# Kernel optimization log

Hardware: AMD Instinct MI355X
Metric: run time of the kernel (lower is better)

Reference implementation:

```python
import jax, jax.numpy as jnp
import numpy as np
from jax.scipy.special import logsumexp

N, K, D = 131072, 256, 32


def setup_inputs() -> dict:
    key = jax.random.key(0)
    k1, k2, k3 = jax.random.split(key, 3)
    points = jax.random.normal(k1, (N, D), dtype=jnp.float32)
    centers = jax.random.uniform(k2, (K, D), dtype=jnp.float32)
    # well-conditioned inverse-sqrt covariances (original used 15*I; scaled to
    # avoid float32 overflow in sqrt(det(covs_inv)) for D=32)
    covs_inv_sqrt = (0.5 * jnp.broadcast_to(jnp.eye(D, dtype=jnp.float32), (K, D, D))
                     + 0.02 * jax.random.normal(k3, (K, D, D), dtype=jnp.float32))
    weights = jnp.ones((K,), dtype=jnp.float32)
    threshold = jnp.zeros((1,), dtype=jnp.float32)
    return {"points": points, "centers": centers,
            "covs_inv_sqrt": covs_inv_sqrt, "weights": weights,
            "threshold": threshold}


def reference(points, centers, covs_inv_sqrt, weights, threshold):
    # refresh(): equal_clusters=True branch
    w = jnp.abs(weights)
    center_prs = w / (w.sum() + 1e-30)                       # [K]
    covs_inv = jnp.einsum('kde,kfe->kdf', covs_inv_sqrt, covs_inv_sqrt)  # [K,D,D]
    coefs = center_prs * jnp.sqrt(jnp.linalg.det(covs_inv))  # [K]

    # pairwise weighted sqdist: q_ij = (x_i - c_j)^T A_j (x_i - c_j)
    B = covs_inv.reshape(K, D * D)                           # [K, D*D]
    X2 = (points[:, :, None] * points[:, None, :]).reshape(N, D * D)  # [N, D*D]
    t_xAx = X2 @ B.T                                         # [N, K]
    m = jnp.einsum('kde,ke->kd', covs_inv, centers)          # A_j c_j, [K,D]
    t_xAc = points @ m.T                                     # [N, K]
    t_cAc = jnp.einsum('kd,kd->k', m, centers)               # [K]
    d_ij = -0.5 * (t_xAx - 2.0 * t_xAc + t_cAc[None, :])     # [N, K]

    # weighted logsumexp over centers, then subtract threshold
    ll = logsumexp(d_ij, axis=1, b=coefs[None, :])           # [N]
    return ll[:, None] - threshold[0]                        # [N, 1]
```

## Files before the change

### kernel.cpp

```cpp
#include <hip/hip_runtime.h>
#include <math.h>

#define NPTS 131072
#define KCOMP 256
#define DIM 32
#define NREAL 560
#define NCH 18
#define PSIF_BYTES 294912
#define WS_NEED (PSIF_BYTES + KCOMP * 4)

typedef __attribute__((ext_vector_type(8))) short short8;
typedef __attribute__((ext_vector_type(16))) float f32x16;

__device__ __forceinline__ unsigned short f2bf(float v) {
    unsigned u = __float_as_uint(v);
    u += 0x7fffu + ((u >> 16) & 1u);
    return (unsigned short)(u >> 16);
}

__device__ __forceinline__ unsigned pkbf(float lo, float hi) {
#if __has_builtin(__builtin_amdgcn_perm)
    const unsigned a = __float_as_uint(hi) + 0x8000u;
    const unsigned b = __float_as_uint(lo) + 0x8000u;
    return __builtin_amdgcn_perm(a, b, 0x07060302u);
#else
    return (unsigned)f2bf(lo) | ((unsigned)f2bf(hi) << 16);
#endif
}

__device__ __forceinline__ void dma16(const uint4* g, uint4* s) {
    __builtin_amdgcn_global_load_lds(
        (const __attribute__((address_space(1))) void*)g,
        (__attribute__((address_space(3))) void*)s, 16, 0, 0);
}

constexpr int PfxT(int d) { return 32 * d - (d * (d - 1)) / 2; }
constexpr int rowT(int p) { int d = 0; while (d < 31 && PfxT(d + 1) <= p) ++d; return d; }
constexpr int colT(int p) { return rowT(p) + (p - PfxT(rowT(p))); }

template<int P, int J>
__device__ __forceinline__ float genOne(const float (&x)[DIM]) {
    constexpr int p = P + J;
    if constexpr (p >= NREAL) {
        return 0.f;
    } else if constexpr (p >= 528) {
        return x[p - 528];
    } else {
        constexpr int d = rowT(p);
        constexpr int f = colT(p);
        static_assert(d >= 0 && d < 32 && f >= d && f < 32, "bad feature map");
        return x[d] * x[f];
    }
}

__global__ __launch_bounds__(256) void gmm_pre(
    const float* __restrict__ S,
    const float* __restrict__ centers,
    const float* __restrict__ weights,
    unsigned short* __restrict__ PsiF,
    float* __restrict__ kc2)
{
    __shared__ float Sl[DIM][DIM + 1];
    __shared__ float As[DIM][DIM + 1];
    __shared__ float cl[DIM], ml[DIM];
    __shared__ float red[256];

    const int k = blockIdx.x, tid = threadIdx.x;

    for (int idx = tid; idx < DIM * DIM; idx += 256)
        Sl[idx >> 5][idx & 31] = S[(size_t)k * DIM * DIM + idx];
    if (tid < DIM) cl[tid] = centers[k * DIM + tid];
    __syncthreads();

    for (int idx = tid; idx < DIM * DIM; idx += 256) {
        const int d = idx >> 5, f = idx & 31;
        float a = 0.f;
#pragma unroll
        for (int e = 0; e < DIM; ++e) a = fmaf(Sl[d][e], Sl[f][e], a);
        As[d][f] = a;
    }
    __syncthreads();

    if (tid < DIM) {
        float mv = 0.f;
#pragma unroll
        for (int f = 0; f < DIM; ++f) mv = fmaf(As[tid][f], cl[f], mv);
        ml[tid] = mv;
    }
    __syncthreads();

    for (int p = tid; p < NREAL; p += 256) {
        float val;
        if (p < 528) {
            int d = 0, pr = 0;
            while (pr + (32 - d) <= p) { pr += (32 - d); ++d; }
            const int f = d + (p - pr);
            val = (f == d) ? -0.5f * As[d][d] : -As[d][f];
        } else {
            val = ml[p - 528];
        }
        const int c = p >> 6, kk = p & 63;
        const int s = kk >> 4, qq = (kk >> 3) & 1, j = kk & 7;
        const int ct = k >> 5, ll = qq * 32 + (k & 31);
        const int g = c * 2048 + (s * 8 + ct) * 64 + ll;
        PsiF[(size_t)g * 8 + j] = f2bf(val);
    }

    red[tid] = fabsf(weights[tid]);
    __syncthreads();
    for (int off = 128; off > 0; off >>= 1) {
        if (tid < off) red[tid] += red[tid + off];
        __syncthreads();
    }
    const float wsum = red[0];

    for (int j = 0; j < DIM - 1; ++j) {
        const float inv = 1.0f / As[j][j];
        for (int idx = tid; idx < DIM * DIM; idx += 256) {
            const int r = idx >> 5, c = idx & 31;
            if (r > j && c > j)
                As[r][c] = fmaf(-As[r][j] * inv, As[j][c], As[r][c]);
        }
        __syncthreads();
    }

    if (tid < DIM) red[tid] = __logf(As[tid][tid]);
    __syncthreads();
    if (tid == 0) {
        float sl = 0.f;
        for (int j = 0; j < DIM; ++j) sl += red[j];
        float cac = 0.f;
        for (int d2 = 0; d2 < DIM; ++d2) cac = fmaf(ml[d2], cl[d2], cac);
        kc2[k] = __logf(fabsf(weights[k])) - __logf(wsum + 1e-30f)
               + 0.5f * sl - 0.5f * cac;
    }
}

template<int P>
__device__ __forceinline__ void genQuad(const float (&x)[DIM], float* v) {
    v[0] = genOne<P, 0>(x);
    v[1] = genOne<P, 1>(x);
    v[2] = genOne<P, 2>(x);
    v[3] = genOne<P, 3>(x);
}

template<int CH, int SS>
__device__ __forceinline__ void genSite(const float (&x)[DIM], uint4* base,
                                        int rbg, int r32) {
    float v[8];
    genQuad<CH * 32 + SS * 8>(x, v);
    genQuad<CH * 32 + SS * 8 + 4>(x, v + 4);
    uint4 u;
    u.x = pkbf(v[0], v[1]);
    u.y = pkbf(v[2], v[3]);
    u.z = pkbf(v[4], v[5]);
    u.w = pkbf(v[6], v[7]);
    base[(SS >> 1) * 256 + rbg * 64 + (SS & 1) * 32 + r32] = u;
}

template<int CH>
__device__ __forceinline__ void genChunk(const float (&x)[DIM], uint4* sA4,
                                         int q, int rbg, int r32) {
    uint4* base = sA4 + (CH & 1) * 512;
    if (q == 0) {
        genSite<CH, 0>(x, base, rbg, r32);
        if constexpr (CH < 17) genSite<CH, 2>(x, base, rbg, r32);
    } else {
        genSite<CH, 1>(x, base, rbg, r32);
        if constexpr (CH < 17) genSite<CH, 3>(x, base, rbg, r32);
    }
}

template<int C>
__device__ __forceinline__ void doChunk(const float (&x)[DIM],
    uint4* sA4, uint4* sB4, const uint4* __restrict__ PsiF4,
    f32x16 (&acc0)[4], f32x16 (&acc1)[4],
    int l, int w, int q, int rbg, int r32, int r0, int c0)
{

    if constexpr (C + 1 < NCH) {
        constexpr int NI = (C + 1 == 17) ? 2 : 4;
        const uint4* src = PsiF4 + (C + 1) * 1024 + w * 64 + l;
        uint4* dst = sB4 + ((C + 1) & 1) * 1024 + w * 64 + l;
#pragma unroll
        for (int i = 0; i < NI; ++i) dma16(src + i * 256, dst + i * 256);
    }

    if constexpr (C + 1 < NCH) genChunk<C + 1>(x, sA4, q, rbg, r32);

    constexpr int NS = (C < 17) ? 2 : 1;
    const uint4* aa = sA4 + (C & 1) * 512;
    const uint4* bb = sB4 + (C & 1) * 1024;
#pragma unroll
    for (int s = 0; s < NS; ++s) {
        short8 a0 = __builtin_bit_cast(short8, aa[(s * 4 + r0) * 64 + l]);
        short8 a1 = __builtin_bit_cast(short8, aa[(s * 4 + r0 + 1) * 64 + l]);
#pragma unroll
        for (int j = 0; j < 4; ++j) {
            short8 b = __builtin_bit_cast(short8, bb[(s * 8 + c0 + j) * 64 + l]);
            acc0[j] = __builtin_amdgcn_mfma_f32_32x32x16_bf16(a0, b, acc0[j], 0, 0, 0);
            acc1[j] = __builtin_amdgcn_mfma_f32_32x32x16_bf16(a1, b, acc1[j], 0, 0, 0);
        }
    }

    __syncthreads();
}

__device__ __forceinline__ void epiHalf(const f32x16 (&acc)[4], const float (&kcv)[4],
    int rblock, int l, int whalf, float (*sM)[2], float (*sS)[2])
{
#pragma unroll
    for (int rg = 0; rg < 16; ++rg) {
        float vals[4], m = -INFINITY;
#pragma unroll
        for (int j = 0; j < 4; ++j) { vals[j] = acc[j][rg] + kcv[j]; m = fmaxf(m, vals[j]); }
#pragma unroll
        for (int mask = 1; mask < 32; mask <<= 1) m = fmaxf(m, __shfl_xor(m, mask, 64));
        float sv = 0.f;
#pragma unroll
        for (int j = 0; j < 4; ++j) sv += __expf(vals[j] - m);
#pragma unroll
        for (int mask = 1; mask < 32; mask <<= 1) sv += __shfl_xor(sv, mask, 64);
        if ((l & 31) == 0) {
            const int R = rblock * 32 + (rg & 3) + 8 * (rg >> 2) + 4 * (l >> 5);
            sM[R][whalf] = m; sS[R][whalf] = sv;
        }
    }
}

__global__ __launch_bounds__(256, 2) void gmm_mfma(
    const float* __restrict__ points,
    const unsigned short* __restrict__ PsiF,
    const float* __restrict__ kc2,
    const float* __restrict__ thr,
    float* __restrict__ out)
{
    __shared__ uint4 sA4[1024];
    __shared__ uint4 sB4[2048];
    float (*sM)[2] = (float (*)[2])sA4;
    float (*sS)[2] = (float (*)[2])(sA4 + 64);

    const int t = threadIdx.x;
    const int w = t >> 6, l = t & 63;
    const int row = t & 127, q = t >> 7;
    const int rbg = row >> 5, r32 = row & 31;
    const int r0 = (w >> 1) * 2, c0 = (w & 1) * 4;

    const uint4* PsiF4 = (const uint4*)PsiF;

    {
        const uint4* src = PsiF4 + w * 64 + l;
        uint4* dst = sB4 + w * 64 + l;
#pragma unroll
        for (int i = 0; i < 4; ++i) dma16(src + i * 256, dst + i * 256);
    }

    float x[DIM];
    const float4* px = (const float4*)(points + ((size_t)blockIdx.x * 128 + row) * DIM);
#pragma unroll
    for (int j2 = 0; j2 < 8; ++j2) {
        float4 v = px[j2];
        x[4 * j2 + 0] = v.x; x[4 * j2 + 1] = v.y;
        x[4 * j2 + 2] = v.z; x[4 * j2 + 3] = v.w;
    }

    f32x16 acc0[4], acc1[4];
#pragma unroll
    for (int j = 0; j < 4; ++j)
#pragma unroll
        for (int r = 0; r < 16; ++r) { acc0[j][r] = 0.f; acc1[j][r] = 0.f; }

    genChunk<0>(x, sA4, q, rbg, r32);
    __syncthreads();

    doChunk<0>(x, sA4, sB4, PsiF4, acc0, acc1, l, w, q, rbg, r32, r0, c0);
    doChunk<1>(x, sA4, sB4, PsiF4, acc0, acc1, l, w, q, rbg, r32, r0, c0);
    doChunk<2>(x, sA4, sB4, PsiF4, acc0, acc1, l, w, q, rbg, r32, r0, c0);
    doChunk<3>(x, sA4, sB4, PsiF4, acc0, acc1, l, w, q, rbg, r32, r0, c0);
    doChunk<4>(x, sA4, sB4, PsiF4, acc0, acc1, l, w, q, rbg, r32, r0, c0);
    doChunk<5>(x, sA4, sB4, PsiF4, acc0, acc1, l, w, q, rbg, r32, r0, c0);
    doChunk<6>(x, sA4, sB4, PsiF4, acc0, acc1, l, w, q, rbg, r32, r0, c0);
    doChunk<7>(x, sA4, sB4, PsiF4, acc0, acc1, l, w, q, rbg, r32, r0, c0);
    doChunk<8>(x, sA4, sB4, PsiF4, acc0, acc1, l, w, q, rbg, r32, r0, c0);
    doChunk<9>(x, sA4, sB4, PsiF4, acc0, acc1, l, w, q, rbg, r32, r0, c0);
    doChunk<10>(x, sA4, sB4, PsiF4, acc0, acc1, l, w, q, rbg, r32, r0, c0);
    doChunk<11>(x, sA4, sB4, PsiF4, acc0, acc1, l, w, q, rbg, r32, r0, c0);
    doChunk<12>(x, sA4, sB4, PsiF4, acc0, acc1, l, w, q, rbg, r32, r0, c0);
    doChunk<13>(x, sA4, sB4, PsiF4, acc0, acc1, l, w, q, rbg, r32, r0, c0);
    doChunk<14>(x, sA4, sB4, PsiF4, acc0, acc1, l, w, q, rbg, r32, r0, c0);
    doChunk<15>(x, sA4, sB4, PsiF4, acc0, acc1, l, w, q, rbg, r32, r0, c0);
    doChunk<16>(x, sA4, sB4, PsiF4, acc0, acc1, l, w, q, rbg, r32, r0, c0);
    doChunk<17>(x, sA4, sB4, PsiF4, acc0, acc1, l, w, q, rbg, r32, r0, c0);

    float kcv[4];
#pragma unroll
    for (int j = 0; j < 4; ++j) kcv[j] = kc2[(c0 + j) * 32 + (l & 31)];

    epiHalf(acc0, kcv, r0,     l, w & 1, sM, sS);
    epiHalf(acc1, kcv, r0 + 1, l, w & 1, sM, sS);
    __syncthreads();

    if (t < 128) {
        const float m0 = sM[t][0], m1 = sM[t][1];
        const float M = fmaxf(m0, m1);
        const float Sv = sS[t][0] * __expf(m0 - M) + sS[t][1] * __expf(m1 - M);
        out[(size_t)blockIdx.x * 128 + t] = M + __logf(Sv) - thr[0];
    }
}

extern "C" void kernel_launch(void* const* d_in, const int* in_sizes, int n_in,
                              void* d_out, int out_size, void* d_ws, size_t ws_size,
                              hipStream_t stream) {
    const float* points  = (const float*)d_in[0];
    const float* centers = (const float*)d_in[1];
    const float* covs    = (const float*)d_in[2];
    const float* weights = (const float*)d_in[3];
    const float* thr     = (const float*)d_in[4];
    float* out = (float*)d_out;

    unsigned short* PsiF = (unsigned short*)d_ws;
    float* kc2 = (float*)((char*)d_ws + PSIF_BYTES);

    gmm_pre<<<KCOMP, 256, 0, stream>>>(covs, centers, weights, PsiF, kc2);
    gmm_mfma<<<NPTS / 128, 256, 0, stream>>>(points, PsiF, kc2, thr, out);
}
```

Measured before the change: 147.3 us.

## Double threads per block to split MFMA row blocks across eight waves

Launches 512 threads per block instead of 256. Each of the eight waves now owns one 32-row block with a single accumulator set, where before four waves each held two. Feature generation is spread over four thread quarters, and the B-tile DMA is split across more threads. This halves per-thread accumulator registers and work so more waves can be resident to hide latency, at the cost of more threads per barrier and reloading the same B fragments in more waves.

```diff
diff --git a/kernel.cpp b/kernel.cpp
--- a/kernel.cpp
+++ b/kernel.cpp
@@ -162,28 +162,30 @@
 __device__ __forceinline__ void genChunk(const float (&x)[DIM], uint4* sA4,
                                          int q, int rbg, int r32) {
     uint4* base = sA4 + (CH & 1) * 512;
-    if (q == 0) {
-        genSite<CH, 0>(x, base, rbg, r32);
-        if constexpr (CH < 17) genSite<CH, 2>(x, base, rbg, r32);
+    if constexpr (CH < 17) {
+        if (q == 0)      genSite<CH, 0>(x, base, rbg, r32);
+        else if (q == 1) genSite<CH, 1>(x, base, rbg, r32);
+        else if (q == 2) genSite<CH, 2>(x, base, rbg, r32);
+        else             genSite<CH, 3>(x, base, rbg, r32);
     } else {
-        genSite<CH, 1>(x, base, rbg, r32);
-        if constexpr (CH < 17) genSite<CH, 3>(x, base, rbg, r32);
+        if (q == 0)      genSite<CH, 0>(x, base, rbg, r32);
+        else if (q == 1) genSite<CH, 1>(x, base, rbg, r32);
     }
 }
 
 template<int C>
 __device__ __forceinline__ void doChunk(const float (&x)[DIM],
     uint4* sA4, uint4* sB4, const uint4* __restrict__ PsiF4,
-    f32x16 (&acc0)[4], f32x16 (&acc1)[4],
-    int l, int w, int q, int rbg, int r32, int r0, int c0)
+    f32x16 (&acc)[4],
+    int l, int w, int q, int rbg, int r32, int rb, int c0)
 {
 
     if constexpr (C + 1 < NCH) {
-        constexpr int NI = (C + 1 == 17) ? 2 : 4;
+        constexpr int NI = (C + 1 == 17) ? 1 : 2;
         const uint4* src = PsiF4 + (C + 1) * 1024 + w * 64 + l;
         uint4* dst = sB4 + ((C + 1) & 1) * 1024 + w * 64 + l;
 #pragma unroll
-        for (int i = 0; i < NI; ++i) dma16(src + i * 256, dst + i * 256);
+        for (int i = 0; i < NI; ++i) dma16(src + i * 512, dst + i * 512);
     }
 
     if constexpr (C + 1 < NCH) genChunk<C + 1>(x, sA4, q, rbg, r32);
@@ -193,13 +195,11 @@
     const uint4* bb = sB4 + (C & 1) * 1024;
 #pragma unroll
     for (int s = 0; s < NS; ++s) {
-        short8 a0 = __builtin_bit_cast(short8, aa[(s * 4 + r0) * 64 + l]);
-        short8 a1 = __builtin_bit_cast(short8, aa[(s * 4 + r0 + 1) * 64 + l]);
+        short8 a = __builtin_bit_cast(short8, aa[(s * 4 + rb) * 64 + l]);
 #pragma unroll
         for (int j = 0; j < 4; ++j) {
             short8 b = __builtin_bit_cast(short8, bb[(s * 8 + c0 + j) * 64 + l]);
-            acc0[j] = __builtin_amdgcn_mfma_f32_32x32x16_bf16(a0, b, acc0[j], 0, 0, 0);
-            acc1[j] = __builtin_amdgcn_mfma_f32_32x32x16_bf16(a1, b, acc1[j], 0, 0, 0);
+            acc[j] = __builtin_amdgcn_mfma_f32_32x32x16_bf16(a, b, acc[j], 0, 0, 0);
         }
     }
 
@@ -228,7 +228,7 @@
     }
 }
 
-__global__ __launch_bounds__(256, 2) void gmm_mfma(
+__global__ __launch_bounds__(512, 4) void gmm_mfma(
     const float* __restrict__ points,
     const unsigned short* __restrict__ PsiF,
     const float* __restrict__ kc2,
@@ -244,15 +244,15 @@
     const int w = t >> 6, l = t & 63;
     const int row = t & 127, q = t >> 7;
     const int rbg = row >> 5, r32 = row & 31;
-    const int r0 = (w >> 1) * 2, c0 = (w & 1) * 4;
+    const int rb = w >> 1, c0 = (w & 1) * 4;
 
     const uint4* PsiF4 = (const uint4*)PsiF;
 
     {
         const uint4* src = PsiF4 + w * 64 + l;
         uint4* dst = sB4 + w * 64 + l;
-#pragma unroll
-        for (int i = 0; i < 4; ++i) dma16(src + i * 256, dst + i * 256);
+        dma16(src, dst);
+        dma16(src + 512, dst + 512);
     }
 
     float x[DIM];
@@ -264,40 +264,39 @@
         x[4 * j2 + 2] = v.z; x[4 * j2 + 3] = v.w;
     }
 
-    f32x16 acc0[4], acc1[4];
+    f32x16 acc[4];
 #pragma unroll
     for (int j = 0; j < 4; ++j)
 #pragma unroll
-        for (int r = 0; r < 16; ++r) { acc0[j][r] = 0.f; acc1[j][r] = 0.f; }
+        for (int r = 0; r < 16; ++r) acc[j][r] = 0.f;
 
     genChunk<0>(x, sA4, q, rbg, r32);
     __syncthreads();
 
-    doChunk<0>(x, sA4, sB4, PsiF4, acc0, acc1, l, w, q, rbg, r32, r0, c0);
-    doChunk<1>(x, sA4, sB4, PsiF4, acc0, acc1, l, w, q, rbg, r32, r0, c0);
-    doChunk<2>(x, sA4, sB4, PsiF4, acc0, acc1, l, w, q, rbg, r32, r0, c0);
-    doChunk<3>(x, sA4, sB4, PsiF4, acc0, acc1, l, w, q, rbg, r32, r0, c0);
-    doChunk<4>(x, sA4, sB4, PsiF4, acc0, acc1, l, w, q, rbg, r32, r0, c0);
-    doChunk<5>(x, sA4, sB4, PsiF4, acc0, acc1, l, w, q, rbg, r32, r0, c0);
-    doChunk<6>(x, sA4, sB4, PsiF4, acc0, acc1, l, w, q, rbg, r32, r0, c0);
-    doChunk<7>(x, sA4, sB4, PsiF4, acc0, acc1, l, w, q, rbg, r32, r0, c0);
-    doChunk<8>(x, sA4, sB4, PsiF4, acc0, acc1, l, w, q, rbg, r32, r0, c0);
-    doChunk<9>(x, sA4, sB4, PsiF4, acc0, acc1, l, w, q, rbg, r32, r0, c0);
-    doChunk<10>(x, sA4, sB4, PsiF4, acc0, acc1, l, w, q, rbg, r32, r0, c0);
-    doChunk<11>(x, sA4, sB4, PsiF4, acc0, acc1, l, w, q, rbg, r32, r0, c0);
-    doChunk<12>(x, sA4, sB4, PsiF4, acc0, acc1, l, w, q, rbg, r32, r0, c0);
-    doChunk<13>(x, sA4, sB4, PsiF4, acc0, acc1, l, w, q, rbg, r32, r0, c0);
-    doChunk<14>(x, sA4, sB4, PsiF4, acc0, acc1, l, w, q, rbg, r32, r0, c0);
-    doChunk<15>(x, sA4, sB4, PsiF4, acc0, acc1, l, w, q, rbg, r32, r0, c0);
-    doChunk<16>(x, sA4, sB4, PsiF4, acc0, acc1, l, w, q, rbg, r32, r0, c0);
-    doChunk<17>(x, sA4, sB4, PsiF4, acc0, acc1, l, w, q, rbg, r32, r0, c0);
+    doChunk<0>(x, sA4, sB4, PsiF4, acc, l, w, q, rbg, r32, rb, c0);
+    doChunk<1>(x, sA4, sB4, PsiF4, acc, l, w, q, rbg, r32, rb, c0);
+    doChunk<2>(x, sA4, sB4, PsiF4, acc, l, w, q, rbg, r32, rb, c0);
+    doChunk<3>(x, sA4, sB4, PsiF4, acc, l, w, q, rbg, r32, rb, c0);
+    doChunk<4>(x, sA4, sB4, PsiF4, acc, l, w, q, rbg, r32, rb, c0);
+    doChunk<5>(x, sA4, sB4, PsiF4, acc, l, w, q, rbg, r32, rb, c0);
+    doChunk<6>(x, sA4, sB4, PsiF4, acc, l, w, q, rbg, r32, rb, c0);
+    doChunk<7>(x, sA4, sB4, PsiF4, acc, l, w, q, rbg, r32, rb, c0);
+    doChunk<8>(x, sA4, sB4, PsiF4, acc, l, w, q, rbg, r32, rb, c0);
+    doChunk<9>(x, sA4, sB4, PsiF4, acc, l, w, q, rbg, r32, rb, c0);
+    doChunk<10>(x, sA4, sB4, PsiF4, acc, l, w, q, rbg, r32, rb, c0);
+    doChunk<11>(x, sA4, sB4, PsiF4, acc, l, w, q, rbg, r32, rb, c0);
+    doChunk<12>(x, sA4, sB4, PsiF4, acc, l, w, q, rbg, r32, rb, c0);
+    doChunk<13>(x, sA4, sB4, PsiF4, acc, l, w, q, rbg, r32, rb, c0);
+    doChunk<14>(x, sA4, sB4, PsiF4, acc, l, w, q, rbg, r32, rb, c0);
+    doChunk<15>(x, sA4, sB4, PsiF4, acc, l, w, q, rbg, r32, rb, c0);
+    doChunk<16>(x, sA4, sB4, PsiF4, acc, l, w, q, rbg, r32, rb, c0);
+    doChunk<17>(x, sA4, sB4, PsiF4, acc, l, w, q, rbg, r32, rb, c0);
 
     float kcv[4];
 #pragma unroll
     for (int j = 0; j < 4; ++j) kcv[j] = kc2[(c0 + j) * 32 + (l & 31)];
 
-    epiHalf(acc0, kcv, r0,     l, w & 1, sM, sS);
-    epiHalf(acc1, kcv, r0 + 1, l, w & 1, sM, sS);
+    epiHalf(acc, kcv, rb, l, w & 1, sM, sS);
     __syncthreads();
 
     if (t < 128) {
@@ -322,5 +321,5 @@
     float* kc2 = (float*)((char*)d_ws + PSIF_BYTES);
 
     gmm_pre<<<KCOMP, 256, 0, stream>>>(covs, centers, weights, PsiF, kc2);
-    gmm_mfma<<<NPTS / 128, 256, 0, stream>>>(points, PsiF, kc2, thr, out);
-}
+    gmm_mfma<<<NPTS / 128, 512, 0, stream>>>(points, PsiF, kc2, thr, out);
+}
```

After: 139.3 us. -5.4%, faster.
